# Kernel optimization log

Measured on AMD Instinct MI355X. Metric: run time of the kernel, lower is better.

## Reference

```python
import jax, jax.numpy as jnp
import numpy as np

N_NODES = 262144
D = 256

def setup_inputs() -> dict:
    key = jax.random.key(0)
    k1, k2, k3 = jax.random.split(key, 3)
    # Xavier-ish scale for weights
    bb_feats = jax.random.normal(k1, (N_NODES, D), dtype=jnp.float32)
    W1 = jax.random.normal(k2, (D, D), dtype=jnp.float32) * (1.0 / np.sqrt(D))
    b1 = jnp.zeros((D,), dtype=jnp.float32)
    W2 = jax.random.normal(k3, (9, D), dtype=jnp.float32) * (1.0 / np.sqrt(D))
    b2 = jnp.zeros((9,), dtype=jnp.float32)
    return {"bb_feats": bb_feats, "W1": W1, "b1": b1, "W2": W2, "b2": b2}

def _special_procrustes(M):
    # Project each 3x3 matrix onto SO(3): R = U diag(1,1,sign(det(U V^T))) V^T
    U, s, Vt = jnp.linalg.svd(M, full_matrices=False)
    d = jnp.sign(jnp.linalg.det(U) * jnp.linalg.det(Vt))  # [...,]
    ones = jnp.ones_like(d)
    col_scale = jnp.stack([ones, ones, d], axis=-1)  # scale last column of U
    return jnp.einsum('nij,nj,njk->nik', U, col_scale, Vt)

def reference(bb_feats, W1, b1, W2, b2):
    # 2-layer MLP head: Linear -> GELU (exact erf) -> Linear to 9
    h = jax.nn.gelu(bb_feats @ W1.T + b1, approximate=False)
    raw = (h @ W2.T + b2).reshape(-1, 3, 3)  # [N, 3, 3]
    return _special_procrustes(raw)
```

## Files before the change

kernel.cpp:

```cpp
#include <hip/hip_runtime.h>
#include <math.h>

#define NN 262144
#define DD 256

typedef __attribute__((ext_vector_type(8))) short bf16x8;
typedef __attribute__((ext_vector_type(4))) float f32x4;

#define MFMA __builtin_amdgcn_mfma_f32_16x16x32_bf16

union U8 { bf16x8 v; unsigned int u[4]; };

__device__ __forceinline__ int swzf(int row, int k) {
  return (row << 8) + ((((k >> 2) ^ (row & 7)) << 2) | (k & 3));
}

__device__ __forceinline__ void split2(float a0, float a1,
                                       unsigned int& ph, unsigned int& pm, unsigned int& pl) {
  unsigned int u0 = __float_as_uint(a0), u1 = __float_as_uint(a1);
  ph = __builtin_amdgcn_perm(u1, u0, 0x07060302u);
  float h0 = __uint_as_float(u0 & 0xffff0000u);
  float h1 = __uint_as_float(u1 & 0xffff0000u);
  float r0 = a0 - h0, r1 = a1 - h1;
  unsigned int v0 = __float_as_uint(r0), v1 = __float_as_uint(r1);
  pm = __builtin_amdgcn_perm(v1, v0, 0x07060302u);
  float m0 = __uint_as_float(v0 & 0xffff0000u);
  float m1 = __uint_as_float(v1 & 0xffff0000u);
  float s0 = r0 - m0, s1 = r1 - m1;
  pl = __builtin_amdgcn_perm(__float_as_uint(s1), __float_as_uint(s0), 0x07060302u);
}

__global__ void prep_kernel(const float* __restrict__ W1,
                            unsigned short* __restrict__ wa,
                            unsigned short* __restrict__ wb,
                            unsigned short* __restrict__ wc) {
  int t = blockIdx.x * 256 + threadIdx.x;
  float v = W1[t];
  unsigned int uv = __float_as_uint(v);
  float hi = __uint_as_float(uv & 0xffff0000u);
  float r1 = v - hi;
  unsigned int u1 = __float_as_uint(r1);
  float mi = __uint_as_float(u1 & 0xffff0000u);
  float r2 = r1 - mi;
  unsigned int u2 = __float_as_uint(r2);
  wa[t] = (unsigned short)(uv >> 16);
  wb[t] = (unsigned short)(u1 >> 16);
  wc[t] = (unsigned short)(u2 >> 16);
}

__global__ __launch_bounds__(256, 2) void mlp_kernel(
    const float* __restrict__ A, const float* __restrict__ b1,
    const float* __restrict__ b2, const float* __restrict__ W2,
    const unsigned short* __restrict__ w1a, const unsigned short* __restrict__ w1b,
    const unsigned short* __restrict__ w1c, float* __restrict__ Mout)
{
  __shared__ float sA[64 * 256];
  __shared__ float sMp[4 * 64 * 12];
  const int tid  = threadIdx.x;
  const int lane = tid & 63;
  const int wv   = tid >> 6;
  const int n0   = blockIdx.x * 64;

  const float4* A4 = (const float4*)(A + (size_t)n0 * DD);
  #pragma unroll
  for (int it = 0; it < 16; ++it) {
    int f   = (it << 8) + tid;
    int row = f >> 6;
    int kc  = (f & 63) << 2;
    float4 v = A4[f];
    *(float4*)&sA[swzf(row, kc)] = v;
  }
  __syncthreads();

  const int m  = lane & 15;
  const int g  = lane >> 4;
  const int kq = g << 3;

  f32x4 acc[4][4];
  #pragma unroll
  for (int r = 0; r < 4; ++r)
    #pragma unroll
    for (int c = 0; c < 4; ++c)
      acc[r][c] = (f32x4){0.f, 0.f, 0.f, 0.f};

  int boff[4];
  #pragma unroll
  for (int c = 0; c < 4; ++c) boff[c] = (wv * 64 + c * 16 + m) * DD + kq;

  #pragma unroll
  for (int ks = 0; ks < 8; ++ks) {
    bf16x8 Ba[4], Bb[4], Bc[4];
    #pragma unroll
    for (int c = 0; c < 4; ++c) {
      Ba[c] = *(const bf16x8*)(w1a + boff[c] + ks * 32);
      Bb[c] = *(const bf16x8*)(w1b + boff[c] + ks * 32);
      Bc[c] = *(const bf16x8*)(w1c + boff[c] + ks * 32);
    }
    U8 Aa[4], Ab[4], Ac[4];
    #pragma unroll
    for (int r = 0; r < 4; ++r) {
      int row = r * 16 + m;
      int k0  = ks * 32 + kq;
      float4 p = *(const float4*)&sA[swzf(row, k0)];
      float4 q = *(const float4*)&sA[swzf(row, k0 + 4)];
      split2(p.x, p.y, Aa[r].u[0], Ab[r].u[0], Ac[r].u[0]);
      split2(p.z, p.w, Aa[r].u[1], Ab[r].u[1], Ac[r].u[1]);
      split2(q.x, q.y, Aa[r].u[2], Ab[r].u[2], Ac[r].u[2]);
      split2(q.z, q.w, Aa[r].u[3], Ab[r].u[3], Ac[r].u[3]);
    }
    #pragma unroll
    for (int r = 0; r < 4; ++r)
      #pragma unroll
      for (int c = 0; c < 4; ++c) {
        f32x4 t;
        t = MFMA(Ac[r].v, Ba[c], acc[r][c], 0, 0, 0);
        t = MFMA(Ab[r].v, Bb[c], t, 0, 0, 0);
        t = MFMA(Aa[r].v, Bc[c], t, 0, 0, 0);
        t = MFMA(Ab[r].v, Ba[c], t, 0, 0, 0);
        t = MFMA(Aa[r].v, Bb[c], t, 0, 0, 0);
        acc[r][c] = MFMA(Aa[r].v, Ba[c], t, 0, 0, 0);
      }
  }
  __syncthreads();

  const int rowq = g << 2;
  #pragma unroll
  for (int c = 0; c < 4; ++c) {
    int j = wv * 64 + c * 16 + m;
    float bias = b1[j];
    #pragma unroll
    for (int r = 0; r < 4; ++r) {
      #pragma unroll
      for (int ri = 0; ri < 4; ++ri) {
        float x  = acc[r][c][ri] + bias;
        float gl = 0.5f * x * (1.f + erff(x * 0.70710678118654752f));
        sA[swzf(r * 16 + rowq + ri, j)] = gl;
      }
    }
  }
  __syncthreads();

  float accj[9];
  #pragma unroll
  for (int j = 0; j < 9; ++j) accj[j] = 0.f;
  int kbase = __builtin_amdgcn_readfirstlane(wv << 6);
  const float* w2k = W2 + kbase;
  #pragma unroll
  for (int kk = 0; kk < 64; kk += 4) {
    float4 h4 = *(const float4*)&sA[swzf(lane, kbase + kk)];
    #pragma unroll
    for (int j = 0; j < 9; ++j) {
      const float* wj = w2k + j * DD + kk;
      accj[j] = fmaf(h4.x, wj[0],
                fmaf(h4.y, wj[1],
                fmaf(h4.z, wj[2],
                fmaf(h4.w, wj[3], accj[j]))));
    }
  }
  #pragma unroll
  for (int j = 0; j < 9; ++j) sMp[(wv * 64 + lane) * 12 + j] = accj[j];
  __syncthreads();

  for (int o = tid; o < 576; o += 256) {
    int row = o / 9, j = o - row * 9;
    float s = sMp[(row) * 12 + j] + sMp[(64 + row) * 12 + j] +
              sMp[(128 + row) * 12 + j] + sMp[(192 + row) * 12 + j] + b2[j];
    Mout[(size_t)(n0 + row) * 9 + j] = s;
  }
}

template <int P, int Q>
__device__ __forceinline__ void jrot(float Aq[4][4], float V[4][4]) {
  float apq = Aq[P][Q];
  float d   = Aq[Q][Q] - Aq[P][P];
  float sq  = sqrtf(d * d + 4.f * apq * apq);
  float den = fmaxf(fabsf(d) + sq, 1e-35f);
  float tt  = 2.f * apq * copysignf(1.f, d) / den;
  float c   = rsqrtf(1.f + tt * tt);
  float s   = tt * c;
  float app = Aq[P][P], aqq = Aq[Q][Q];
  Aq[P][P] = app - tt * apq;
  Aq[Q][Q] = aqq + tt * apq;
  Aq[P][Q] = 0.f; Aq[Q][P] = 0.f;
  #pragma unroll
  for (int r = 0; r < 4; ++r) {
    if (r == P || r == Q) continue;
    float arp = Aq[r][P], arq = Aq[r][Q];
    Aq[r][P] = Aq[P][r] = c * arp - s * arq;
    Aq[r][Q] = Aq[Q][r] = s * arp + c * arq;
  }
  #pragma unroll
  for (int i = 0; i < 4; ++i) {
    float vp = V[i][P], vq = V[i][Q];
    V[i][P] = c * vp - s * vq;
    V[i][Q] = s * vp + c * vq;
  }
}

__device__ __forceinline__ double det3(double a, double b, double c,
                                       double d, double e, double f,
                                       double g, double h, double i) {
  return a * (e * i - f * h) - b * (d * i - f * g) + c * (d * h - e * g);
}

__global__ __launch_bounds__(256) void procrustes_kernel(const float* __restrict__ M,
                                                         float* __restrict__ out) {
  int t = blockIdx.x * 256 + threadIdx.x;
  const float* mp = M + (size_t)t * 9;
  float m00 = mp[0], m01 = mp[1], m02 = mp[2];
  float m10 = mp[3], m11 = mp[4], m12 = mp[5];
  float m20 = mp[6], m21 = mp[7], m22 = mp[8];

  float Aq[4][4], V[4][4];
  Aq[0][0] =  m00 + m11 + m22;
  Aq[1][1] =  m00 - m11 - m22;
  Aq[2][2] = -m00 + m11 - m22;
  Aq[3][3] = -m00 - m11 + m22;
  Aq[0][1] = Aq[1][0] = m21 - m12;
  Aq[0][2] = Aq[2][0] = m02 - m20;
  Aq[0][3] = Aq[3][0] = m10 - m01;
  Aq[1][2] = Aq[2][1] = m01 + m10;
  Aq[1][3] = Aq[3][1] = m02 + m20;
  Aq[2][3] = Aq[3][2] = m12 + m21;
  #pragma unroll
  for (int i = 0; i < 4; ++i)
    #pragma unroll
    for (int j = 0; j < 4; ++j)
      V[i][j] = (i == j) ? 1.f : 0.f;

  #pragma unroll
  for (int sweep = 0; sweep < 5; ++sweep) {
    jrot<0,1>(Aq, V); jrot<0,2>(Aq, V); jrot<0,3>(Aq, V);
    jrot<1,2>(Aq, V); jrot<1,3>(Aq, V); jrot<2,3>(Aq, V);
  }

  float bv = Aq[0][0];
  float qw = V[0][0], qx = V[1][0], qy = V[2][0], qz = V[3][0];
  #define PICK(K) if (Aq[K][K] > bv) { bv = Aq[K][K]; qw = V[0][K]; qx = V[1][K]; qy = V[2][K]; qz = V[3][K]; }
  PICK(1) PICK(2) PICK(3)
  #undef PICK

  double d00 = (double)m00, d01 = (double)m01, d02 = (double)m02;
  double d10 = (double)m10, d11 = (double)m11, d12 = (double)m12;
  double d20 = (double)m20, d21 = (double)m21, d22 = (double)m22;
  double Nd[4][4];
  Nd[0][0] =  d00 + d11 + d22;
  Nd[1][1] =  d00 - d11 - d22;
  Nd[2][2] = -d00 + d11 - d22;
  Nd[3][3] = -d00 - d11 + d22;
  Nd[0][1] = Nd[1][0] = d21 - d12;
  Nd[0][2] = Nd[2][0] = d02 - d20;
  Nd[0][3] = Nd[3][0] = d10 - d01;
  Nd[1][2] = Nd[2][1] = d01 + d10;
  Nd[1][3] = Nd[3][1] = d02 + d20;
  Nd[2][3] = Nd[3][2] = d12 + d21;

  double qd[4] = {(double)qw, (double)qx, (double)qy, (double)qz};
  double nn = qd[0]*qd[0] + qd[1]*qd[1] + qd[2]*qd[2] + qd[3]*qd[3];
  double Nq[4];
  #pragma unroll
  for (int i = 0; i < 4; ++i)
    Nq[i] = Nd[i][0]*qd[0] + Nd[i][1]*qd[1] + Nd[i][2]*qd[2] + Nd[i][3]*qd[3];
  double sig = (qd[0]*Nq[0] + qd[1]*Nq[1] + qd[2]*Nq[2] + qd[3]*Nq[3]) / nn;

  double Ad[4][4];
  #pragma unroll
  for (int i = 0; i < 4; ++i)
    #pragma unroll
    for (int j = 0; j < 4; ++j)
      Ad[i][j] = Nd[i][j] - (i == j ? sig : 0.0);

  double y[4];
  #pragma unroll
  for (int i = 0; i < 4; ++i) {
    double yi = 0.0;
    #pragma unroll
    for (int j = 0; j < 4; ++j) {
      const int r0 = (i == 0) ? 1 : 0, r1 = (i <= 1) ? 2 : 1, r2 = (i <= 2) ? 3 : 2;
      const int c0 = (j == 0) ? 1 : 0, c1 = (j <= 1) ? 2 : 1, c2 = (j <= 2) ? 3 : 2;
      double mnr = det3(Ad[r0][c0], Ad[r0][c1], Ad[r0][c2],
                        Ad[r1][c0], Ad[r1][c1], Ad[r1][c2],
                        Ad[r2][c0], Ad[r2][c1], Ad[r2][c2]);
      double s = ((i + j) & 1) ? -mnr : mnr;
      yi += s * qd[j];
    }
    y[i] = yi;
  }
  double yn = y[0]*y[0] + y[1]*y[1] + y[2]*y[2] + y[3]*y[3];
  if (!(yn > 1e-280)) { y[0] = qd[0]; y[1] = qd[1]; y[2] = qd[2]; y[3] = qd[3]; yn = nn; }
  double inv = 1.0 / sqrt(yn);
  double w = y[0]*inv, x = y[1]*inv, yv = y[2]*inv, z = y[3]*inv;

  double xx = x*x, yy = yv*yv, zz = z*z;
  double xy = x*yv, xz = x*z, yz = yv*z;
  double wx = w*x, wy = w*yv, wz = w*z;

  float* op = out + (size_t)t * 9;
  op[0] = (float)(1.0 - 2.0*(yy + zz));
  op[1] = (float)(2.0*(xy - wz));
  op[2] = (float)(2.0*(xz + wy));
  op[3] = (float)(2.0*(xy + wz));
  op[4] = (float)(1.0 - 2.0*(xx + zz));
  op[5] = (float)(2.0*(yz - wx));
  op[6] = (float)(2.0*(xz - wy));
  op[7] = (float)(2.0*(yz + wx));
  op[8] = (float)(1.0 - 2.0*(xx + yy));
}

extern "C" void kernel_launch(void* const* d_in, const int* in_sizes, int n_in,
                              void* d_out, int out_size, void* d_ws, size_t ws_size,
                              hipStream_t stream) {
  const float* bb = (const float*)d_in[0];
  const float* W1 = (const float*)d_in[1];
  const float* b1 = (const float*)d_in[2];
  const float* W2 = (const float*)d_in[3];
  const float* b2 = (const float*)d_in[4];
  float* out = (float*)d_out;
  char* ws = (char*)d_ws;
  unsigned short* w1a = (unsigned short*)(ws);
  unsigned short* w1b = (unsigned short*)(ws + 131072);
  unsigned short* w1c = (unsigned short*)(ws + 262144);
  float* Mbuf = (float*)(ws + 393216);

  hipLaunchKernelGGL(prep_kernel, dim3(256), dim3(256), 0, stream, W1, w1a, w1b, w1c);
  hipLaunchKernelGGL(mlp_kernel, dim3(NN / 64), dim3(256), 0, stream,
                     bb, b1, b2, W2, w1a, w1b, w1c, Mbuf);
  hipLaunchKernelGGL(procrustes_kernel, dim3(NN / 256), dim3(256), 0, stream, Mbuf, out);
}
```

Baseline: 587.4 us.

## Use fp16 hi/lo split with 3 MFMAs and fast erf GELU

Replaces the 6-MFMA bf16x3 emulation of the fp32 first GEMM with a two-term fp16 split (hi plus scaled lo), using 3 fp16 MFMAs per tile. A is converted once while staging into shared memory instead of per fragment. The block is doubled to 512 threads with half the columns per wave, GELU uses a polynomial erf approximation, and the second layer uses a shuffle reduction in place of a shared-memory reduction. This cuts MFMA count and conversion work, at the cost of lower accuracy: fp16 range limits and the approximate erf.

```diff
diff --git a/kernel.cpp b/kernel.cpp
--- a/kernel.cpp
+++ b/kernel.cpp
@@ -4,58 +4,57 @@
 #define NN 262144
 #define DD 256
 
-typedef __attribute__((ext_vector_type(8))) short bf16x8;
+typedef __attribute__((ext_vector_type(8))) _Float16 h16x8;
 typedef __attribute__((ext_vector_type(4))) float f32x4;
 
-#define MFMA __builtin_amdgcn_mfma_f32_16x16x32_bf16
-
-union U8 { bf16x8 v; unsigned int u[4]; };
-
+#define MFMA16 __builtin_amdgcn_mfma_f32_16x16x32_f16
+
+__device__ __forceinline__ int swz16(int row, int k) {
+  return (row << 8) + ((((k >> 3) ^ (row & 7)) << 3) | (k & 7));
+}
 __device__ __forceinline__ int swzf(int row, int k) {
   return (row << 8) + ((((k >> 2) ^ (row & 7)) << 2) | (k & 3));
 }
 
-__device__ __forceinline__ void split2(float a0, float a1,
-                                       unsigned int& ph, unsigned int& pm, unsigned int& pl) {
-  unsigned int u0 = __float_as_uint(a0), u1 = __float_as_uint(a1);
-  ph = __builtin_amdgcn_perm(u1, u0, 0x07060302u);
-  float h0 = __uint_as_float(u0 & 0xffff0000u);
-  float h1 = __uint_as_float(u1 & 0xffff0000u);
-  float r0 = a0 - h0, r1 = a1 - h1;
-  unsigned int v0 = __float_as_uint(r0), v1 = __float_as_uint(r1);
-  pm = __builtin_amdgcn_perm(v1, v0, 0x07060302u);
-  float m0 = __uint_as_float(v0 & 0xffff0000u);
-  float m1 = __uint_as_float(v1 & 0xffff0000u);
-  float s0 = r0 - m0, s1 = r1 - m1;
-  pl = __builtin_amdgcn_perm(__float_as_uint(s1), __float_as_uint(s0), 0x07060302u);
+__device__ __forceinline__ void hsplit(float a, unsigned short& hb, unsigned short& lb) {
+  _Float16 h = (_Float16)a;
+  float r = a - (float)h;
+  _Float16 l = (_Float16)(r * 4096.f);
+  hb = __builtin_bit_cast(unsigned short, h);
+  lb = __builtin_bit_cast(unsigned short, l);
+}
+
+__device__ __forceinline__ float gelu_fast(float x) {
+  float z  = fabsf(x) * 0.70710678118654752f;
+  float t  = __builtin_amdgcn_rcpf(fmaf(0.3275911f, z, 1.f));
+  float P  = t * fmaf(t, fmaf(t, fmaf(t, fmaf(t, 1.061405429f, -1.453152027f),
+                                      1.421413741f), -0.284496736f), 0.254829592f);
+  float E  = __builtin_amdgcn_exp2f(-1.442695041f * z * z);
+  float er = fmaf(-P, E, 1.f);
+  return 0.5f * x * (1.f + copysignf(er, x));
 }
 
 __global__ void prep_kernel(const float* __restrict__ W1,
-                            unsigned short* __restrict__ wa,
-                            unsigned short* __restrict__ wb,
-                            unsigned short* __restrict__ wc) {
+                            unsigned short* __restrict__ wh,
+                            unsigned short* __restrict__ wl) {
   int t = blockIdx.x * 256 + threadIdx.x;
-  float v = W1[t];
-  unsigned int uv = __float_as_uint(v);
-  float hi = __uint_as_float(uv & 0xffff0000u);
-  float r1 = v - hi;
-  unsigned int u1 = __float_as_uint(r1);
-  float mi = __uint_as_float(u1 & 0xffff0000u);
-  float r2 = r1 - mi;
-  unsigned int u2 = __float_as_uint(r2);
-  wa[t] = (unsigned short)(uv >> 16);
-  wb[t] = (unsigned short)(u1 >> 16);
-  wc[t] = (unsigned short)(u2 >> 16);
-}
-
-__global__ __launch_bounds__(256, 2) void mlp_kernel(
+  unsigned short hb, lb;
+  hsplit(W1[t], hb, lb);
+  wh[t] = hb;
+  wl[t] = lb;
+}
+
+__global__ __launch_bounds__(512, 4) void mlp_kernel(
     const float* __restrict__ A, const float* __restrict__ b1,
     const float* __restrict__ b2, const float* __restrict__ W2,
-    const unsigned short* __restrict__ w1a, const unsigned short* __restrict__ w1b,
-    const unsigned short* __restrict__ w1c, float* __restrict__ Mout)
+    const unsigned short* __restrict__ w1h, const unsigned short* __restrict__ w1l,
+    float* __restrict__ Mout)
 {
-  __shared__ float sA[64 * 256];
-  __shared__ float sMp[4 * 64 * 12];
+  __shared__ unsigned short sbuf[32768];
+  unsigned short* sH = sbuf;
+  unsigned short* sL = sbuf + 16384;
+  float* sF = (float*)sbuf;
+
   const int tid  = threadIdx.x;
   const int lane = tid & 63;
   const int wv   = tid >> 6;
@@ -63,12 +62,19 @@
 
   const float4* A4 = (const float4*)(A + (size_t)n0 * DD);
   #pragma unroll
-  for (int it = 0; it < 16; ++it) {
-    int f   = (it << 8) + tid;
+  for (int it = 0; it < 8; ++it) {
+    int f   = (it << 9) + tid;
     int row = f >> 6;
     int kc  = (f & 63) << 2;
     float4 v = A4[f];
-    *(float4*)&sA[swzf(row, kc)] = v;
+    ushort4 hv, lv;
+    hsplit(v.x, hv.x, lv.x);
+    hsplit(v.y, hv.y, lv.y);
+    hsplit(v.z, hv.z, lv.z);
+    hsplit(v.w, hv.w, lv.w);
+    int idx = swz16(row, kc);
+    *(ushort4*)&sH[idx] = hv;
+    *(ushort4*)&sL[idx] = lv;
   }
   __syncthreads();
 
@@ -76,96 +82,79 @@
   const int g  = lane >> 4;
   const int kq = g << 3;
 
-  f32x4 acc[4][4];
+  f32x4 acc0[4][2], acc1[4][2];
   #pragma unroll
   for (int r = 0; r < 4; ++r)
     #pragma unroll
-    for (int c = 0; c < 4; ++c)
-      acc[r][c] = (f32x4){0.f, 0.f, 0.f, 0.f};
-
-  int boff[4];
-  #pragma unroll
-  for (int c = 0; c < 4; ++c) boff[c] = (wv * 64 + c * 16 + m) * DD + kq;
+    for (int c = 0; c < 2; ++c) {
+      acc0[r][c] = (f32x4){0.f, 0.f, 0.f, 0.f};
+      acc1[r][c] = (f32x4){0.f, 0.f, 0.f, 0.f};
+    }
+
+  const int bcol0 = (wv * 32 + m) * DD + kq;
+  const int bcol1 = (wv * 32 + 16 + m) * DD + kq;
 
   #pragma unroll
   for (int ks = 0; ks < 8; ++ks) {
-    bf16x8 Ba[4], Bb[4], Bc[4];
-    #pragma unroll
-    for (int c = 0; c < 4; ++c) {
-      Ba[c] = *(const bf16x8*)(w1a + boff[c] + ks * 32);
-      Bb[c] = *(const bf16x8*)(w1b + boff[c] + ks * 32);
-      Bc[c] = *(const bf16x8*)(w1c + boff[c] + ks * 32);
-    }
-    U8 Aa[4], Ab[4], Ac[4];
+    h16x8 Bh[2], Bl[2];
+    Bh[0] = *(const h16x8*)(w1h + bcol0 + ks * 32);
+    Bh[1] = *(const h16x8*)(w1h + bcol1 + ks * 32);
+    Bl[0] = *(const h16x8*)(w1l + bcol0 + ks * 32);
+    Bl[1] = *(const h16x8*)(w1l + bcol1 + ks * 32);
     #pragma unroll
     for (int r = 0; r < 4; ++r) {
-      int row = r * 16 + m;
-      int k0  = ks * 32 + kq;
-      float4 p = *(const float4*)&sA[swzf(row, k0)];
-      float4 q = *(const float4*)&sA[swzf(row, k0 + 4)];
-      split2(p.x, p.y, Aa[r].u[0], Ab[r].u[0], Ac[r].u[0]);
-      split2(p.z, p.w, Aa[r].u[1], Ab[r].u[1], Ac[r].u[1]);
-      split2(q.x, q.y, Aa[r].u[2], Ab[r].u[2], Ac[r].u[2]);
-      split2(q.z, q.w, Aa[r].u[3], Ab[r].u[3], Ac[r].u[3]);
-    }
-    #pragma unroll
-    for (int r = 0; r < 4; ++r)
+      int ai = swz16(r * 16 + m, ks * 32 + kq);
+      h16x8 Ah = *(const h16x8*)&sH[ai];
+      h16x8 Al = *(const h16x8*)&sL[ai];
       #pragma unroll
-      for (int c = 0; c < 4; ++c) {
-        f32x4 t;
-        t = MFMA(Ac[r].v, Ba[c], acc[r][c], 0, 0, 0);
-        t = MFMA(Ab[r].v, Bb[c], t, 0, 0, 0);
-        t = MFMA(Aa[r].v, Bc[c], t, 0, 0, 0);
-        t = MFMA(Ab[r].v, Ba[c], t, 0, 0, 0);
-        t = MFMA(Aa[r].v, Bb[c], t, 0, 0, 0);
-        acc[r][c] = MFMA(Aa[r].v, Ba[c], t, 0, 0, 0);
+      for (int c = 0; c < 2; ++c) {
+        acc1[r][c] = MFMA16(Al, Bh[c], acc1[r][c], 0, 0, 0);
+        acc1[r][c] = MFMA16(Ah, Bl[c], acc1[r][c], 0, 0, 0);
+        acc0[r][c] = MFMA16(Ah, Bh[c], acc0[r][c], 0, 0, 0);
       }
+    }
   }
   __syncthreads();
 
-  const int rowq = g << 2;
-  #pragma unroll
-  for (int c = 0; c < 4; ++c) {
-    int j = wv * 64 + c * 16 + m;
+  #pragma unroll
+  for (int c = 0; c < 2; ++c) {
+    int j = wv * 32 + c * 16 + m;
     float bias = b1[j];
     #pragma unroll
     for (int r = 0; r < 4; ++r) {
       #pragma unroll
       for (int ri = 0; ri < 4; ++ri) {
-        float x  = acc[r][c][ri] + bias;
-        float gl = 0.5f * x * (1.f + erff(x * 0.70710678118654752f));
-        sA[swzf(r * 16 + rowq + ri, j)] = gl;
+        float x = fmaf(acc1[r][c][ri], 2.44140625e-4f, acc0[r][c][ri]) + bias;
+        sF[swzf(r * 16 + g * 4 + ri, j)] = gelu_fast(x);
       }
     }
   }
   __syncthreads();
 
-  float accj[9];
-  #pragma unroll
-  for (int j = 0; j < 9; ++j) accj[j] = 0.f;
-  int kbase = __builtin_amdgcn_readfirstlane(wv << 6);
-  const float* w2k = W2 + kbase;
-  #pragma unroll
-  for (int kk = 0; kk < 64; kk += 4) {
-    float4 h4 = *(const float4*)&sA[swzf(lane, kbase + kk)];
+  const int rloc = lane >> 3;
+  const int row  = wv * 8 + rloc;
+  const int kc   = (lane & 7) << 5;
+  float aj[9];
+  #pragma unroll
+  for (int j = 0; j < 9; ++j) aj[j] = 0.f;
+  #pragma unroll
+  for (int kk = 0; kk < 32; kk += 4) {
+    float4 h4 = *(const float4*)&sF[swzf(row, kc + kk)];
     #pragma unroll
     for (int j = 0; j < 9; ++j) {
-      const float* wj = w2k + j * DD + kk;
-      accj[j] = fmaf(h4.x, wj[0],
-                fmaf(h4.y, wj[1],
-                fmaf(h4.z, wj[2],
-                fmaf(h4.w, wj[3], accj[j]))));
-    }
-  }
-  #pragma unroll
-  for (int j = 0; j < 9; ++j) sMp[(wv * 64 + lane) * 12 + j] = accj[j];
-  __syncthreads();
-
-  for (int o = tid; o < 576; o += 256) {
-    int row = o / 9, j = o - row * 9;
-    float s = sMp[(row) * 12 + j] + sMp[(64 + row) * 12 + j] +
-              sMp[(128 + row) * 12 + j] + sMp[(192 + row) * 12 + j] + b2[j];
-    Mout[(size_t)(n0 + row) * 9 + j] = s;
+      float4 w = *(const float4*)(W2 + j * DD + kc + kk);
+      aj[j] = fmaf(h4.x, w.x, fmaf(h4.y, w.y, fmaf(h4.z, w.z, fmaf(h4.w, w.w, aj[j]))));
+    }
+  }
+  #pragma unroll
+  for (int off = 1; off < 8; off <<= 1)
+    #pragma unroll
+    for (int j = 0; j < 9; ++j)
+      aj[j] += __shfl_xor(aj[j], off, 64);
+  if ((lane & 7) == 0) {
+    float* op = Mout + (size_t)(n0 + row) * 9;
+    #pragma unroll
+    for (int j = 0; j < 9; ++j) op[j] = aj[j] + b2[j];
   }
 }
 
@@ -317,13 +306,12 @@
   const float* b2 = (const float*)d_in[4];
   float* out = (float*)d_out;
   char* ws = (char*)d_ws;
-  unsigned short* w1a = (unsigned short*)(ws);
-  unsigned short* w1b = (unsigned short*)(ws + 131072);
-  unsigned short* w1c = (unsigned short*)(ws + 262144);
-  float* Mbuf = (float*)(ws + 393216);
-
-  hipLaunchKernelGGL(prep_kernel, dim3(256), dim3(256), 0, stream, W1, w1a, w1b, w1c);
-  hipLaunchKernelGGL(mlp_kernel, dim3(NN / 64), dim3(256), 0, stream,
-                     bb, b1, b2, W2, w1a, w1b, w1c, Mbuf);
+  unsigned short* w1h = (unsigned short*)(ws);
+  unsigned short* w1l = (unsigned short*)(ws + 131072);
+  float* Mbuf = (float*)(ws + 262144);
+
+  hipLaunchKernelGGL(prep_kernel, dim3(256), dim3(256), 0, stream, W1, w1h, w1l);
+  hipLaunchKernelGGL(mlp_kernel, dim3(NN / 64), dim3(512), 0, stream,
+                     bb, b1, b2, W2, w1h, w1l, Mbuf);
   hipLaunchKernelGGL(procrustes_kernel, dim3(NN / 256), dim3(256), 0, stream, Mbuf, out);
 }
```

After: 769.0 us. +30.9%, slower.
